# Kernel optimization log

Measured on AMD Instinct MI355X. Metric: run time of the kernel, lower is better.

The kernel has to match this reference:

```python
import jax, jax.numpy as jnp
import numpy as np

NEG_BIG = -9e15
ALPHA = 0.2  # LeakyReLU negative slope


def setup_inputs() -> dict:
    key = jax.random.key(0)
    k1, k2, k3, k4 = jax.random.split(key, 4)
    B, N, Fin, Fout = 4, 2048, 128, 128
    h = jax.random.normal(k1, (B, N, Fin), dtype=jnp.float32)
    adj = jax.random.randint(k2, (N, N), 0, 2, dtype=jnp.int32)
    W = jax.random.normal(k3, (Fin, Fout), dtype=jnp.float32) * 0.1
    a = jax.random.normal(k4, (2 * Fout, 1), dtype=jnp.float32) * 0.1
    return {"h": h, "adj": adj, "W": W, "a": a}


def reference(h, adj, W, a):
    # Wh: [B, N, Fout]
    Wh = jnp.einsum('bnf,fo->bno', h, W)
    Fout = W.shape[1]
    a1 = a[:Fout, 0]   # attends to source i
    a2 = a[Fout:, 0]   # attends to target j
    # Decomposed form of leakyrelu(cat([Wh_i, Wh_j]) @ a):
    # e_ij = leakyrelu(a1.Wh_i + a2.Wh_j)  -> [B, N, N]
    f1 = Wh @ a1  # [B, N]
    f2 = Wh @ a2  # [B, N]
    e = jax.nn.leaky_relu(f1[:, :, None] + f2[:, None, :], negative_slope=ALPHA)
    attention = jnp.where(adj[None, :, :] > 0, e, jnp.float32(NEG_BIG))
    attention = jax.nn.softmax(attention, axis=2)
    # dropout is identity in eval mode
    h_prime = jnp.einsum('bij,bjo->bio', attention, Wh)
    return h_prime
```

## Files before the change

kernel.cpp:

```cpp
#include <hip/hip_runtime.h>

#define BB 4
#define NN 2048
#define FF 128
#define NP 2176
#define ALPHA 0.2f
#define SHIFT_C 16.0f

typedef short bf16x8 __attribute__((ext_vector_type(8)));
typedef float f32x4 __attribute__((ext_vector_type(4)));
typedef unsigned u32;

__device__ inline short f2bf(float f) {
    union { float f; unsigned u; } v; v.f = f;
    unsigned r = (v.u + 0x7FFFu + ((v.u >> 16) & 1u)) >> 16;
    return (short)r;
}
__device__ inline float bf2f(short s) {
    union { float f; unsigned u; } v;
    v.u = ((unsigned)(unsigned short)s) << 16;
    return v.f;
}

__global__ __launch_bounds__(256) void k_wh(const float* __restrict__ h,
                                            const float* __restrict__ W,
                                            const float* __restrict__ a,
                                            const int* __restrict__ adj,
                                            short* __restrict__ WhHiT,
                                            short* __restrict__ WhLoT,
                                            float* __restrict__ f1,
                                            float* __restrict__ f2,
                                            u32* __restrict__ adjp) {
    __shared__ float Wa[2 * FF];
    __shared__ float hs[16 * 132];
    int tid = threadIdx.x;
    int r0 = blockIdx.x * 16;

    {
        int fin = tid & 127;
        const float* av = (tid < 128) ? a : (a + FF);
        const float* wr = W + (size_t)fin * FF;
        float s = 0.f;
        for (int o = 0; o < FF; o += 4) {
            float4 wv = *(const float4*)(wr + o);
            float4 avv = *(const float4*)(av + o);
            s += wv.x * avv.x + wv.y * avv.y + wv.z * avv.z + wv.w * avv.w;
        }
        Wa[(tid < 128 ? 0 : FF) + fin] = s;
    }
    {
        const float4* src = (const float4*)(h + (size_t)r0 * FF);
        float4* dst = (float4*)hs;
        dst[tid] = src[tid];
        dst[256 + tid] = src[256 + tid];
    }
    {
        int g = blockIdx.x * 256 + tid;
        int row = g >> 6, wd = g & 63;
        const int4* ar = (const int4*)(adj + (size_t)row * NN + wd * 32);
        u32 word = 0;
#pragma unroll
        for (int q = 0; q < 8; ++q) {
            int4 v = ar[q];
            word |= (u32)(v.x > 0) << (q * 4);
            word |= (u32)(v.y > 0) << (q * 4 + 1);
            word |= (u32)(v.z > 0) << (q * 4 + 2);
            word |= (u32)(v.w > 0) << (q * 4 + 3);
        }
        adjp[row * 64 + wd] = word;
    }
    __syncthreads();

    {
        int w = tid >> 6, lane = tid & 63;
        float wa1_0 = Wa[lane], wa1_1 = Wa[lane + 64];
        float wa2_0 = Wa[FF + lane], wa2_1 = Wa[FF + lane + 64];
        for (int rr = 0; rr < 4; ++rr) {
            int rloc = w * 4 + rr;
            int row = r0 + rloc;
            float x0 = hs[rloc * FF + lane], x1 = hs[rloc * FF + lane + 64];
            float s1 = x0 * wa1_0 + x1 * wa1_1;
            float s2 = x0 * wa2_0 + x1 * wa2_1;
#pragma unroll
            for (int m = 32; m >= 1; m >>= 1) {
                s1 += __shfl_xor(s1, m, 64);
                s2 += __shfl_xor(s2, m, 64);
            }
            if (lane == 0) { f1[row] = s1; f2[row] = s2; }
        }
    }

    int f4 = (tid & 31) * 4;
    int rg = tid >> 5;
    float acc[2][4];
#pragma unroll
    for (int rr = 0; rr < 2; ++rr)
#pragma unroll
        for (int cc = 0; cc < 4; ++cc) acc[rr][cc] = 0.f;

    for (int k0 = 0; k0 < FF; k0 += 4) {
        float4 wv[4];
#pragma unroll
        for (int kk = 0; kk < 4; ++kk)
            wv[kk] = *(const float4*)(W + (size_t)(k0 + kk) * FF + f4);
        float4 hv[2];
#pragma unroll
        for (int rr = 0; rr < 2; ++rr)
            hv[rr] = *(const float4*)(hs + (rg * 2 + rr) * FF + k0);
#pragma unroll
        for (int rr = 0; rr < 2; ++rr) {
            float hk[4] = {hv[rr].x, hv[rr].y, hv[rr].z, hv[rr].w};
#pragma unroll
            for (int kk = 0; kk < 4; ++kk) {
                acc[rr][0] += hk[kk] * wv[kk].x;
                acc[rr][1] += hk[kk] * wv[kk].y;
                acc[rr][2] += hk[kk] * wv[kk].z;
                acc[rr][3] += hk[kk] * wv[kk].w;
            }
        }
    }

    __syncthreads();
    {
#pragma unroll
        for (int rr = 0; rr < 2; ++rr)
            *(float4*)(hs + (rg * 2 + rr) * 132 + f4) =
                make_float4(acc[rr][0], acc[rr][1], acc[rr][2], acc[rr][3]);
    }
    __syncthreads();
    {
        int fo = tid >> 1, jh = tid & 1;
        bf16x8 hv_, lv_;
#pragma unroll
        for (int jj = 0; jj < 8; ++jj) {
            float v = hs[(jh * 8 + jj) * 132 + fo];
            short hh = f2bf(v);
            hv_[jj] = hh;
            lv_[jj] = f2bf(v - bf2f(hh));
        }
        int b = r0 >> 11;
        int j0 = (r0 & (NN - 1)) + jh * 8;
        size_t off = (size_t)(b * FF + fo) * NP + j0;
        *(bf16x8*)(WhHiT + off) = hv_;
        *(bf16x8*)(WhLoT + off) = lv_;
    }
}

#define EV(f2v, f1v, wv, bi) ({ float _t = (f1v) + (f2v); float _x = fmaxf(_t, ALPHA * _t); \
    __expf(_x - SHIFT_C) * (float)(((wv) >> (bi)) & 1u); })

#define BUILD_A(Adst, F1V, WV, SP) { \
    float pa, pb; \
    pa = EV(q0.x, F1V, WV, bb + 0); pb = EV(q0.y, F1V, WV, bb + 1); \
    SP += pa + pb; \
    asm("v_cvt_pk_bf16_f32 %0, %1, %2" : "=v"(Adst.u[0]) : "v"(pa), "v"(pb)); \
    pa = EV(q0.z, F1V, WV, bb + 2); pb = EV(q0.w, F1V, WV, bb + 3); \
    SP += pa + pb; \
    asm("v_cvt_pk_bf16_f32 %0, %1, %2" : "=v"(Adst.u[1]) : "v"(pa), "v"(pb)); \
    pa = EV(q1.x, F1V, WV, bb + 4); pb = EV(q1.y, F1V, WV, bb + 5); \
    SP += pa + pb; \
    asm("v_cvt_pk_bf16_f32 %0, %1, %2" : "=v"(Adst.u[2]) : "v"(pa), "v"(pb)); \
    pa = EV(q1.z, F1V, WV, bb + 6); pb = EV(q1.w, F1V, WV, bb + 7); \
    SP += pa + pb; \
    asm("v_cvt_pk_bf16_f32 %0, %1, %2" : "=v"(Adst.u[3]) : "v"(pa), "v"(pb)); }

__global__ __launch_bounds__(512) void k_attn(const short* __restrict__ WhHiT,
                                              const short* __restrict__ WhLoT,
                                              const u32* __restrict__ adjp,
                                              const float* __restrict__ f1,
                                              const float* __restrict__ f2,
                                              float* __restrict__ out) {
    __shared__ __align__(16) char lds[33920];
    float* row_ps = (float*)(lds + 32768);
    float* row_inv = (float*)(lds + 33792);

    int tid = threadIdx.x;
    int w = tid >> 6, lane = tid & 63;
    int blk = blockIdx.x;
    int b = blk >> 8;
    int tile = (blk >> 2) & 63;
    int qt = blk & 3;
    int i0 = tile * 32;

    int r_c = lane & 15, kg = lane >> 4;

    const float* f2b = f2 + b * NN;
    float f10 = f1[b * NN + i0 + r_c];
    float f11 = f1[b * NN + i0 + 16 + r_c];
    const u32* ap0 = adjp + (size_t)(i0 + r_c) * 64;

    const ptrdiff_t dLo = (ptrdiff_t)BB * FF * NP;
    int s0 = w * 8;
    const short* pB0 = WhHiT + (size_t)(b * FF + qt * 32 + 0 * 16 + r_c) * NP + s0 * 32 + kg * 8;
    const short* pB1 = WhHiT + (size_t)(b * FF + qt * 32 + 1 * 16 + r_c) * NP + s0 * 32 + kg * 8;

    f32x4 acc0_0 = {0,0,0,0}, acc0_1 = {0,0,0,0};
    f32x4 acc1_0 = {0,0,0,0}, acc1_1 = {0,0,0,0};
    float sp0 = 0.f, sp1 = 0.f;

#pragma unroll
    for (int s8 = 0; s8 < 8; ++s8) {
        int s = s0 + s8;
        float4 q0 = *(const float4*)(f2b + s * 32 + kg * 8);
        float4 q1 = *(const float4*)(f2b + s * 32 + kg * 8 + 4);
        u32 w0 = ap0[s], w1 = ap0[1024 + s];
        bf16x8 bh0 = *(const bf16x8*)(pB0); bf16x8 bl0 = *(const bf16x8*)(pB0 + dLo);
        bf16x8 bh1 = *(const bf16x8*)(pB1); bf16x8 bl1 = *(const bf16x8*)(pB1 + dLo);

        int bb = kg * 8;
        {
            union { u32 u[4]; bf16x8 v; } A;
            BUILD_A(A, f10, w0, sp0)
            acc0_0 = __builtin_amdgcn_mfma_f32_16x16x32_bf16(A.v, bh0, acc0_0, 0, 0, 0);
            acc0_0 = __builtin_amdgcn_mfma_f32_16x16x32_bf16(A.v, bl0, acc0_0, 0, 0, 0);
            acc1_0 = __builtin_amdgcn_mfma_f32_16x16x32_bf16(A.v, bh1, acc1_0, 0, 0, 0);
            acc1_0 = __builtin_amdgcn_mfma_f32_16x16x32_bf16(A.v, bl1, acc1_0, 0, 0, 0);
        }
        {
            union { u32 u[4]; bf16x8 v; } A;
            BUILD_A(A, f11, w1, sp1)
            acc0_1 = __builtin_amdgcn_mfma_f32_16x16x32_bf16(A.v, bh0, acc0_1, 0, 0, 0);
            acc0_1 = __builtin_amdgcn_mfma_f32_16x16x32_bf16(A.v, bl0, acc0_1, 0, 0, 0);
            acc1_1 = __builtin_amdgcn_mfma_f32_16x16x32_bf16(A.v, bh1, acc1_1, 0, 0, 0);
            acc1_1 = __builtin_amdgcn_mfma_f32_16x16x32_bf16(A.v, bl1, acc1_1, 0, 0, 0);
        }

        pB0 += 32; pB1 += 32;
    }

    sp0 += __shfl_xor(sp0, 16, 64); sp0 += __shfl_xor(sp0, 32, 64);
    sp1 += __shfl_xor(sp1, 16, 64); sp1 += __shfl_xor(sp1, 32, 64);
    if (lane < 16) {
        row_ps[w * 32 + lane] = sp0;
        row_ps[w * 32 + 16 + lane] = sp1;
    }
    {
        char* img = lds + w * 4096;
#define STACC(NI, MI, A) { int ch = (((NI)*16 + r_c) * 8 + (MI)*4 + kg) ^ (r_c & 7); \
                           *(f32x4*)(img + ch * 16) = (A); }
        STACC(0, 0, acc0_0) STACC(0, 1, acc0_1)
        STACC(1, 0, acc1_0) STACC(1, 1, acc1_1)
#undef STACC
    }
    __syncthreads();
    if (tid < 32) {
        float t = 0.f;
#pragma unroll
        for (int ww = 0; ww < 8; ++ww) t += row_ps[ww * 32 + tid];
        row_inv[tid] = 1.0f / t;
    }
    __syncthreads();

    if (lane < 32) {
        int colg = w * 4 + (lane >> 3);
        int rq = lane & 7;
        int ch = (colg * 8 + rq) ^ (colg & 7);
        f32x4 v = {0, 0, 0, 0};
#pragma unroll
        for (int im = 0; im < 8; ++im)
            v += *(const f32x4*)(lds + im * 4096 + ch * 16);
        f32x4 rinv = *(const f32x4*)((char*)row_inv + rq * 16);
        float* ob = out + ((size_t)b * NN + i0 + rq * 4) * FF + qt * 32 + colg;
#pragma unroll
        for (int q = 0; q < 4; ++q)
            ob[(size_t)q * FF] = v[q] * rinv[q];
    }
}

extern "C" void kernel_launch(void* const* d_in, const int* in_sizes, int n_in,
                              void* d_out, int out_size, void* d_ws, size_t ws_size,
                              hipStream_t stream) {
    const float* h   = (const float*)d_in[0];
    const int*   adj = (const int*)d_in[1];
    const float* W   = (const float*)d_in[2];
    const float* a   = (const float*)d_in[3];
    float* out = (float*)d_out;

    short* WhHiT = (short*)d_ws;
    short* WhLoT = WhHiT + (size_t)BB * FF * NP;
    float* f1 = (float*)(WhLoT + (size_t)BB * FF * NP);
    float* f2 = f1 + (size_t)BB * NN;
    u32* adjp = (u32*)(f2 + (size_t)BB * NN);

    k_wh<<<(BB * NN) / 16, 256, 0, stream>>>(h, W, a, adj, WhHiT, WhLoT, f1, f2, adjp);
    k_attn<<<1024, 512, 0, stream>>>(WhHiT, WhLoT, adjp, f1, f2, out);
}
```

Baseline: 129.9 us.

## Double row tile, precompute shifted LeakyReLU terms, compute row sums via MFMA

Each attention block now covers 64 rows instead of 32, so every loaded Wh B-fragment and f2 vector is reused across four row groups and the grid is halved. k_wh precomputes f2-SHIFT and ALPHA*f2-SHIFT, which turns the LeakyReLU into a single max of two adds. The softmax denominator is now accumulated by an extra MFMA against a ones vector instead of scalar adds and shuffles. The costs are more accumulator registers, double the LDS, an extra f2 array load, and bf16 rounding in the row sums.

New measurement: 161.0 us. 1.24x slower.

```diff
diff --git a/kernel.cpp b/kernel.cpp
--- a/kernel.cpp
+++ b/kernel.cpp
@@ -29,7 +29,8 @@
                                             short* __restrict__ WhHiT,
                                             short* __restrict__ WhLoT,
                                             float* __restrict__ f1,
-                                            float* __restrict__ f2,
+                                            float* __restrict__ f2s,
+                                            float* __restrict__ f2a,
                                             u32* __restrict__ adjp) {
     __shared__ float Wa[2 * FF];
     __shared__ float hs[16 * 132];
@@ -86,7 +87,11 @@
                 s1 += __shfl_xor(s1, m, 64);
                 s2 += __shfl_xor(s2, m, 64);
             }
-            if (lane == 0) { f1[row] = s1; f2[row] = s2; }
+            if (lane == 0) {
+                f1[row] = s1;
+                f2s[row] = s2 - SHIFT_C;
+                f2a[row] = ALPHA * s2 - SHIFT_C;
+            }
         }
     }
 
@@ -146,47 +151,49 @@
     }
 }
 
-#define EV(f2v, f1v, wv, bi) ({ float _t = (f1v) + (f2v); float _x = fmaxf(_t, ALPHA * _t); \
-    __expf(_x - SHIFT_C) * (float)(((wv) >> (bi)) & 1u); })
-
-#define BUILD_A(Adst, F1V, WV, SP) { \
+#define EV2(fs, fa, f1v, af1v, wv, bi) ({ \
+    float _x = fmaxf((f1v) + (fs), (af1v) + (fa)); \
+    __expf(_x) * (float)(((wv) >> (bi)) & 1u); })
+
+#define BUILD_A2(Adst, F1V, AF1V, WV) { \
     float pa, pb; \
-    pa = EV(q0.x, F1V, WV, bb + 0); pb = EV(q0.y, F1V, WV, bb + 1); \
-    SP += pa + pb; \
+    pa = EV2(q0s.x, q0a.x, F1V, AF1V, WV, bb + 0); pb = EV2(q0s.y, q0a.y, F1V, AF1V, WV, bb + 1); \
     asm("v_cvt_pk_bf16_f32 %0, %1, %2" : "=v"(Adst.u[0]) : "v"(pa), "v"(pb)); \
-    pa = EV(q0.z, F1V, WV, bb + 2); pb = EV(q0.w, F1V, WV, bb + 3); \
-    SP += pa + pb; \
+    pa = EV2(q0s.z, q0a.z, F1V, AF1V, WV, bb + 2); pb = EV2(q0s.w, q0a.w, F1V, AF1V, WV, bb + 3); \
     asm("v_cvt_pk_bf16_f32 %0, %1, %2" : "=v"(Adst.u[1]) : "v"(pa), "v"(pb)); \
-    pa = EV(q1.x, F1V, WV, bb + 4); pb = EV(q1.y, F1V, WV, bb + 5); \
-    SP += pa + pb; \
+    pa = EV2(q1s.x, q1a.x, F1V, AF1V, WV, bb + 4); pb = EV2(q1s.y, q1a.y, F1V, AF1V, WV, bb + 5); \
     asm("v_cvt_pk_bf16_f32 %0, %1, %2" : "=v"(Adst.u[2]) : "v"(pa), "v"(pb)); \
-    pa = EV(q1.z, F1V, WV, bb + 6); pb = EV(q1.w, F1V, WV, bb + 7); \
-    SP += pa + pb; \
+    pa = EV2(q1s.z, q1a.z, F1V, AF1V, WV, bb + 6); pb = EV2(q1s.w, q1a.w, F1V, AF1V, WV, bb + 7); \
     asm("v_cvt_pk_bf16_f32 %0, %1, %2" : "=v"(Adst.u[3]) : "v"(pa), "v"(pb)); }
 
-__global__ __launch_bounds__(512) void k_attn(const short* __restrict__ WhHiT,
-                                              const short* __restrict__ WhLoT,
-                                              const u32* __restrict__ adjp,
-                                              const float* __restrict__ f1,
-                                              const float* __restrict__ f2,
-                                              float* __restrict__ out) {
-    __shared__ __align__(16) char lds[33920];
-    float* row_ps = (float*)(lds + 32768);
-    float* row_inv = (float*)(lds + 33792);
+__global__ __launch_bounds__(512, 4) void k_attn(const short* __restrict__ WhHiT,
+                                                 const short* __restrict__ WhLoT,
+                                                 const u32* __restrict__ adjp,
+                                                 const float* __restrict__ f1,
+                                                 const float* __restrict__ f2s,
+                                                 const float* __restrict__ f2a,
+                                                 float* __restrict__ out) {
+    __shared__ __align__(16) char lds[67840];
+    float* row_ps = (float*)(lds + 65536);
+    float* row_inv = (float*)(lds + 67584);
 
     int tid = threadIdx.x;
     int w = tid >> 6, lane = tid & 63;
     int blk = blockIdx.x;
-    int b = blk >> 8;
-    int tile = (blk >> 2) & 63;
+    int b = blk >> 7;
+    int tile = (blk >> 2) & 31;
     int qt = blk & 3;
-    int i0 = tile * 32;
+    int i0 = tile * 64;
 
     int r_c = lane & 15, kg = lane >> 4;
 
-    const float* f2b = f2 + b * NN;
+    const float* f2sb = f2s + b * NN;
+    const float* f2ab = f2a + b * NN;
     float f10 = f1[b * NN + i0 + r_c];
     float f11 = f1[b * NN + i0 + 16 + r_c];
+    float f12 = f1[b * NN + i0 + 32 + r_c];
+    float f13 = f1[b * NN + i0 + 48 + r_c];
+    float af10 = ALPHA * f10, af11 = ALPHA * f11, af12 = ALPHA * f12, af13 = ALPHA * f13;
     const u32* ap0 = adjp + (size_t)(i0 + r_c) * 64;
 
     const ptrdiff_t dLo = (ptrdiff_t)BB * FF * NP;
@@ -194,23 +201,29 @@
     const short* pB0 = WhHiT + (size_t)(b * FF + qt * 32 + 0 * 16 + r_c) * NP + s0 * 32 + kg * 8;
     const short* pB1 = WhHiT + (size_t)(b * FF + qt * 32 + 1 * 16 + r_c) * NP + s0 * 32 + kg * 8;
 
-    f32x4 acc0_0 = {0,0,0,0}, acc0_1 = {0,0,0,0};
-    f32x4 acc1_0 = {0,0,0,0}, acc1_1 = {0,0,0,0};
-    float sp0 = 0.f, sp1 = 0.f;
+    union { u32 u[4]; bf16x8 v; } ones;
+    ones.u[0] = ones.u[1] = ones.u[2] = ones.u[3] = 0x3F803F80u;
+
+    f32x4 acc0_0 = {0,0,0,0}, acc0_1 = {0,0,0,0}, acc0_2 = {0,0,0,0}, acc0_3 = {0,0,0,0};
+    f32x4 acc1_0 = {0,0,0,0}, acc1_1 = {0,0,0,0}, acc1_2 = {0,0,0,0}, acc1_3 = {0,0,0,0};
+    f32x4 accs0 = {0,0,0,0}, accs1 = {0,0,0,0}, accs2 = {0,0,0,0}, accs3 = {0,0,0,0};
 
 #pragma unroll
     for (int s8 = 0; s8 < 8; ++s8) {
         int s = s0 + s8;
-        float4 q0 = *(const float4*)(f2b + s * 32 + kg * 8);
-        float4 q1 = *(const float4*)(f2b + s * 32 + kg * 8 + 4);
-        u32 w0 = ap0[s], w1 = ap0[1024 + s];
+        float4 q0s = *(const float4*)(f2sb + s * 32 + kg * 8);
+        float4 q1s = *(const float4*)(f2sb + s * 32 + kg * 8 + 4);
+        float4 q0a = *(const float4*)(f2ab + s * 32 + kg * 8);
+        float4 q1a = *(const float4*)(f2ab + s * 32 + kg * 8 + 4);
+        u32 w0 = ap0[s], w1 = ap0[1024 + s], w2 = ap0[2048 + s], w3 = ap0[3072 + s];
         bf16x8 bh0 = *(const bf16x8*)(pB0); bf16x8 bl0 = *(const bf16x8*)(pB0 + dLo);
         bf16x8 bh1 = *(const bf16x8*)(pB1); bf16x8 bl1 = *(const bf16x8*)(pB1 + dLo);
 
         int bb = kg * 8;
         {
             union { u32 u[4]; bf16x8 v; } A;
-            BUILD_A(A, f10, w0, sp0)
+            BUILD_A2(A, f10, af10, w0)
+            accs0  = __builtin_amdgcn_mfma_f32_16x16x32_bf16(A.v, ones.v, accs0, 0, 0, 0);
             acc0_0 = __builtin_amdgcn_mfma_f32_16x16x32_bf16(A.v, bh0, acc0_0, 0, 0, 0);
             acc0_0 = __builtin_amdgcn_mfma_f32_16x16x32_bf16(A.v, bl0, acc0_0, 0, 0, 0);
             acc1_0 = __builtin_amdgcn_mfma_f32_16x16x32_bf16(A.v, bh1, acc1_0, 0, 0, 0);
@@ -218,47 +231,69 @@
         }
         {
             union { u32 u[4]; bf16x8 v; } A;
-            BUILD_A(A, f11, w1, sp1)
+            BUILD_A2(A, f11, af11, w1)
+            accs1  = __builtin_amdgcn_mfma_f32_16x16x32_bf16(A.v, ones.v, accs1, 0, 0, 0);
             acc0_1 = __builtin_amdgcn_mfma_f32_16x16x32_bf16(A.v, bh0, acc0_1, 0, 0, 0);
             acc0_1 = __builtin_amdgcn_mfma_f32_16x16x32_bf16(A.v, bl0, acc0_1, 0, 0, 0);
             acc1_1 = __builtin_amdgcn_mfma_f32_16x16x32_bf16(A.v, bh1, acc1_1, 0, 0, 0);
             acc1_1 = __builtin_amdgcn_mfma_f32_16x16x32_bf16(A.v, bl1, acc1_1, 0, 0, 0);
         }
+        {
+            union { u32 u[4]; bf16x8 v; } A;
+            BUILD_A2(A, f12, af12, w2)
+            accs2  = __builtin_amdgcn_mfma_f32_16x16x32_bf16(A.v, ones.v, accs2, 0, 0, 0);
+            acc0_2 = __builtin_amdgcn_mfma_f32_16x16x32_bf16(A.v, bh0, acc0_2, 0, 0, 0);
+            acc0_2 = __builtin_amdgcn_mfma_f32_16x16x32_bf16(A.v, bl0, acc0_2, 0, 0, 0);
+            acc1_2 = __builtin_amdgcn_mfma_f32_16x16x32_bf16(A.v, bh1, acc1_2, 0, 0, 0);
+            acc1_2 = __builtin_amdgcn_mfma_f32_16x16x32_bf16(A.v, bl1, acc1_2, 0, 0, 0);
+        }
+        {
+            union { u32 u[4]; bf16x8 v; } A;
+            BUILD_A2(A, f13, af13, w3)
+            accs3  = __builtin_amdgcn_mfma_f32_16x16x32_bf16(A.v, ones.v, accs3, 0, 0, 0);
+            acc0_3 = __builtin_amdgcn_mfma_f32_16x16x32_bf16(A.v, bh0, acc0_3, 0, 0, 0);
+            acc0_3 = __builtin_amdgcn_mfma_f32_16x16x32_bf16(A.v, bl0, acc0_3, 0, 0, 0);
+            acc1_3 = __builtin_amdgcn_mfma_f32_16x16x32_bf16(A.v, bh1, acc1_3, 0, 0, 0);
+            acc1_3 = __builtin_amdgcn_mfma_f32_16x16x32_bf16(A.v, bl1, acc1_3, 0, 0, 0);
+        }
 
         pB0 += 32; pB1 += 32;
     }
 
-    sp0 += __shfl_xor(sp0, 16, 64); sp0 += __shfl_xor(sp0, 32, 64);
-    sp1 += __shfl_xor(sp1, 16, 64); sp1 += __shfl_xor(sp1, 32, 64);
-    if (lane < 16) {
-        row_ps[w * 32 + lane] = sp0;
-        row_ps[w * 32 + 16 + lane] = sp1;
-    }
-    {
-        char* img = lds + w * 4096;
-#define STACC(NI, MI, A) { int ch = (((NI)*16 + r_c) * 8 + (MI)*4 + kg) ^ (r_c & 7); \
+    if (r_c == 0) {
+#pragma unroll
+        for (int q = 0; q < 4; ++q) {
+            row_ps[w * 64 +      kg * 4 + q] = accs0[q];
+            row_ps[w * 64 + 16 + kg * 4 + q] = accs1[q];
+            row_ps[w * 64 + 32 + kg * 4 + q] = accs2[q];
+            row_ps[w * 64 + 48 + kg * 4 + q] = accs3[q];
+        }
+    }
+    {
+        char* img = lds + w * 8192;
+#define STACC(NI, MI, A) { int ch = (((NI)*16 + r_c) * 16 + (MI)*4 + kg) ^ (r_c & 7); \
                            *(f32x4*)(img + ch * 16) = (A); }
-        STACC(0, 0, acc0_0) STACC(0, 1, acc0_1)
-        STACC(1, 0, acc1_0) STACC(1, 1, acc1_1)
+        STACC(0, 0, acc0_0) STACC(0, 1, acc0_1) STACC(0, 2, acc0_2) STACC(0, 3, acc0_3)
+        STACC(1, 0, acc1_0) STACC(1, 1, acc1_1) STACC(1, 2, acc1_2) STACC(1, 3, acc1_3)
 #undef STACC
     }
     __syncthreads();
-    if (tid < 32) {
+    if (tid < 64) {
         float t = 0.f;
 #pragma unroll
-        for (int ww = 0; ww < 8; ++ww) t += row_ps[ww * 32 + tid];
+        for (int ww = 0; ww < 8; ++ww) t += row_ps[ww * 64 + tid];
         row_inv[tid] = 1.0f / t;
     }
     __syncthreads();
 
-    if (lane < 32) {
-        int colg = w * 4 + (lane >> 3);
-        int rq = lane & 7;
-        int ch = (colg * 8 + rq) ^ (colg & 7);
+    {
+        int colg = w * 4 + (lane >> 4);
+        int rq = lane & 15;
+        int ch = (colg * 16 + rq) ^ (colg & 7);
         f32x4 v = {0, 0, 0, 0};
 #pragma unroll
         for (int im = 0; im < 8; ++im)
-            v += *(const f32x4*)(lds + im * 4096 + ch * 16);
+            v += *(const f32x4*)(lds + im * 8192 + ch * 16);
         f32x4 rinv = *(const f32x4*)((char*)row_inv + rq * 16);
         float* ob = out + ((size_t)b * NN + i0 + rq * 4) * FF + qt * 32 + colg;
 #pragma unroll
@@ -278,10 +313,11 @@
 
     short* WhHiT = (short*)d_ws;
     short* WhLoT = WhHiT + (size_t)BB * FF * NP;
-    float* f1 = (float*)(WhLoT + (size_t)BB * FF * NP);
-    float* f2 = f1 + (size_t)BB * NN;
-    u32* adjp = (u32*)(f2 + (size_t)BB * NN);
-
-    k_wh<<<(BB * NN) / 16, 256, 0, stream>>>(h, W, a, adj, WhHiT, WhLoT, f1, f2, adjp);
-    k_attn<<<1024, 512, 0, stream>>>(WhHiT, WhLoT, adjp, f1, f2, out);
-}
+    float* f1  = (float*)(WhLoT + (size_t)BB * FF * NP);
+    float* f2s = f1 + (size_t)BB * NN;
+    float* f2a = f2s + (size_t)BB * NN;
+    u32* adjp = (u32*)(f2a + (size_t)BB * NN);
+
+    k_wh<<<(BB * NN) / 16, 256, 0, stream>>>(h, W, a, adj, WhHiT, WhLoT, f1, f2s, f2a, adjp);
+    k_attn<<<512, 512, 0, stream>>>(WhHiT, WhLoT, adjp, f1, f2s, f2a, out);
+}
```
